# Performance work log

Hardware: AMD Instinct MI355X
Metric: run time of the kernel (lower is better)

## Reference

```python
import jax, jax.numpy as jnp
import numpy as np

N = 50000      # nodes
E = 800000     # edges (avg degree 16)
IN = 128       # in_channels
OUT = 128      # out_channels


def setup_inputs() -> dict:
    key = jax.random.key(0)
    k1, k2, k3 = jax.random.split(key, 3)
    x = jax.random.normal(k1, (N, IN), dtype=jnp.float32)
    edge_index = jax.random.randint(k2, (2, E), 0, N, dtype=jnp.int32)
    # GCNConv params: glorot-ish linear weight + zero bias
    W = jax.random.normal(k3, (IN, OUT), dtype=jnp.float32) / np.float32(np.sqrt(IN))
    b = jnp.zeros((OUT,), dtype=jnp.float32)
    return {"x": x, "W": W, "b": b, "edge_index": edge_index}


def reference(x, W, b, edge_index):
    n = x.shape[0]
    src, dst = edge_index[0], edge_index[1]
    # add self loops (GCNConv default add_self_loops=True)
    loop = jnp.arange(n, dtype=edge_index.dtype)
    src = jnp.concatenate([src, loop])
    dst = jnp.concatenate([dst, loop])
    # symmetric normalization: deg^{-1/2}[src] * deg^{-1/2}[dst], deg from dst (flow source_to_target)
    deg = jax.ops.segment_sum(jnp.ones_like(dst, dtype=x.dtype), dst, num_segments=n)
    dinv = jnp.where(deg > 0, jax.lax.rsqrt(jnp.maximum(deg, 1.0)), 0.0)
    norm = dinv[src] * dinv[dst]                     # [E+N]
    xw = x @ W                                       # [N, OUT] dense GEMM first (as GCNConv does)
    msg = xw[src] * norm[:, None]                    # [E+N, OUT] gather + scale
    out = jax.ops.segment_sum(msg, dst, num_segments=n)  # scatter-add aggregate
    return out + b
```

## Files before the change

kernel.cpp:

```cpp
#include <hip/hip_runtime.h>


constexpr int CH = 128;
constexpr int CHUNK = 4096;
constexpr int NCMAX = 256;

typedef __attribute__((ext_vector_type(8))) short short8;
typedef __attribute__((ext_vector_type(4))) float f32x4;

static __device__ __forceinline__ ushort f2bf(float f) {
    unsigned u = __float_as_uint(f);
    u += 0x7fff + ((u >> 16) & 1);
    return (ushort)(u >> 16);
}


__global__ __launch_bounds__(256) void hist_kernel(const int* __restrict__ dst,
                                                   int* __restrict__ h, int E, int nc) {
    __shared__ int hh[NCMAX];
    int t = threadIdx.x, b = blockIdx.x;
    for (int i = t; i < nc; i += 256) hh[i] = 0;
    __syncthreads();
    int s = b * CHUNK, e = min(E, s + CHUNK);
    for (int i = s + t; i < e; i += 256) atomicAdd(&hh[dst[i] >> 8], 1);
    __syncthreads();
    for (int i = t; i < nc; i += 256) h[b * nc + i] = hh[i];
}

__global__ __launch_bounds__(256) void colscan_cols(int* __restrict__ h,
        int* __restrict__ coltot, int nblk, int nc) {
    __shared__ int sm[256];
    int i = blockIdx.x;
    int t = threadIdx.x;
    int v = (t < nblk) ? h[t * nc + i] : 0;
    sm[t] = v;
    __syncthreads();
    #pragma unroll
    for (int d = 1; d < 256; d <<= 1) {
        int u = (t >= d) ? sm[t - d] : 0;
        __syncthreads();
        sm[t] += u;
        __syncthreads();
    }
    if (t < nblk) h[t * nc + i] = sm[t] - v;
    if (t == 255) coltot[i] = sm[255];
}

__global__ __launch_bounds__(256) void scan_bbase(const int* __restrict__ coltot,
        int* __restrict__ bbase, int nc) {
    __shared__ int sm[256];
    int t = threadIdx.x;
    int v = (t < nc) ? coltot[t] : 0;
    sm[t] = v;
    __syncthreads();
    #pragma unroll
    for (int d = 1; d < 256; d <<= 1) {
        int u = (t >= d) ? sm[t - d] : 0;
        __syncthreads();
        sm[t] += u;
        __syncthreads();
    }
    if (t < nc) bbase[t] = sm[t] - v;
    if (t == nc - 1) bbase[nc] = sm[t];
}

__global__ __launch_bounds__(256) void binscatter_kernel(const int* __restrict__ src,
        const int* __restrict__ dst, const int* __restrict__ h,
        const int* __restrict__ bbase, unsigned* __restrict__ ebuf, int E, int nc) {
    __shared__ int cur[NCMAX];
    int t = threadIdx.x, b = blockIdx.x;
    for (int i = t; i < nc; i += 256) cur[i] = h[b * nc + i] + bbase[i];
    __syncthreads();
    int s = b * CHUNK, e = min(E, s + CHUNK);
    for (int i = s + t; i < e; i += 256) {
        int d = dst[i];
        int pos = atomicAdd(&cur[d >> 8], 1);
        ebuf[pos] = (unsigned)src[i] | ((unsigned)(d & 255) << 16);
    }
}

__global__ __launch_bounds__(256) void bucket_csr_kernel(const unsigned* __restrict__ ebuf,
        const int* __restrict__ bbase, int* __restrict__ off, ushort* __restrict__ csr,
        float* __restrict__ dinv, int N) {
    __shared__ int hist[256], cur[256], sc[256];
    int t = threadIdx.x, k = blockIdx.x;
    int s = bbase[k], e = bbase[k + 1];
    hist[t] = 0;
    __syncthreads();
    for (int i = s + t; i < e; i += 256) atomicAdd(&hist[(ebuf[i] >> 16) & 255], 1);
    __syncthreads();
    int v = hist[t];
    sc[t] = v;
    __syncthreads();
    #pragma unroll
    for (int d = 1; d < 256; d <<= 1) {
        int u = (t >= d) ? sc[t - d] : 0;
        __syncthreads();
        sc[t] += u;
        __syncthreads();
    }
    int excl = sc[t] - v;
    int node = k * 256 + t;
    if (node <= N) off[node] = s + excl;
    if (node < N) dinv[node] = rsqrtf((float)(v + 1));
    cur[t] = s + excl;
    __syncthreads();
    for (int i = s + t; i < e; i += 256) {
        unsigned u = ebuf[i];
        int pos = atomicAdd(&cur[(u >> 16) & 255], 1);
        csr[pos] = (ushort)(u & 0xffffu);
    }
}


__global__ void pack_w(const float* __restrict__ W, ushort* __restrict__ Wp) {
    int tid = blockIdx.x * blockDim.x + threadIdx.x;
    if (tid >= 2048) return;
    int col = tid >> 4, chunk = tid & 15;
    ushort tmp[8];
    #pragma unroll
    for (int i = 0; i < 8; ++i)
        tmp[i] = f2bf(W[(size_t)(chunk * 8 + i) * CH + col]);
    int d = col * 16 + (chunk ^ (col & 7));
    *(uint4*)&Wp[(size_t)d * 8] = *(uint4*)tmp;
}


__global__ __launch_bounds__(256) void gemm_mfma(const float* __restrict__ x,
        const ushort* __restrict__ Wp, const float* __restrict__ dinv,
        ushort* __restrict__ xwd, int N) {
    __shared__ alignas(16) ushort Wlds[16384];
    int t = threadIdx.x;
    int wv = t >> 6, l = t & 63;
    int c15 = l & 15, kc = l >> 4;
    int row0 = blockIdx.x * 64 + wv * 16;
    int r = row0 + c15;
    bool valid = r < N;

    short8 af[4];
    #pragma unroll
    for (int ks = 0; ks < 4; ++ks) {
        float4 a0 = make_float4(0.f,0.f,0.f,0.f), a1 = a0;
        if (valid) {
            const float* p = x + (size_t)r * CH + ks * 32 + kc * 8;
            a0 = *(const float4*)p;
            a1 = *(const float4*)(p + 4);
        }
        short8 v;
        v[0]=f2bf(a0.x); v[1]=f2bf(a0.y); v[2]=f2bf(a0.z); v[3]=f2bf(a0.w);
        v[4]=f2bf(a1.x); v[5]=f2bf(a1.y); v[6]=f2bf(a1.z); v[7]=f2bf(a1.w);
        af[ks] = v;
    }

    #pragma unroll
    for (int i = 0; i < 8; ++i) {
        int idx = i * 256 + t;
        *(uint4*)&Wlds[idx * 8] = *(const uint4*)&Wp[idx * 8];
    }
    __syncthreads();

    f32x4 acc[8];
    #pragma unroll
    for (int ct = 0; ct < 8; ++ct) { f32x4 z = {0.f,0.f,0.f,0.f}; acc[ct] = z; }

    int swz = l & 7;
    #pragma unroll
    for (int ks = 0; ks < 4; ++ks) {
        #pragma unroll
        for (int ct = 0; ct < 8; ++ct) {
            int col = ct * 16 + c15;
            int idx16 = (col * 16 + ks * 4 + kc) ^ swz;
            short8 bfrag = *(const short8*)&Wlds[idx16 * 8];
            acc[ct] = __builtin_amdgcn_mfma_f32_16x16x32_bf16(af[ks], bfrag, acc[ct], 0, 0, 0);
        }
    }

    float dv[4];
    #pragma unroll
    for (int rr = 0; rr < 4; ++rr) {
        int row = row0 + kc * 4 + rr;
        dv[rr] = (row < N) ? dinv[row] : 0.f;
    }
    __syncthreads();

    ushort* bw = Wlds + wv * 2048;
    #pragma unroll
    for (int ct = 0; ct < 8; ++ct) {
        #pragma unroll
        for (int rr = 0; rr < 4; ++rr) {
            int row_local = kc * 4 + rr;
            bw[row_local * CH + ct * 16 + c15] = f2bf(acc[ct][rr] * dv[rr]);
        }
    }
    #pragma unroll
    for (int p = 0; p < 4; ++p) {
        int row_local = p * 4 + kc;
        int row = row0 + row_local;
        if (row < N) {
            uint4 vv = *(const uint4*)&bw[row_local * CH + c15 * 8];
            *(uint4*)&xwd[(size_t)row * CH + c15 * 8] = vv;
        }
    }
}


#define ACC8(v)                                    \
    acc[0] += __uint_as_float((v).x << 16);        \
    acc[1] += __uint_as_float((v).x & 0xffff0000u);\
    acc[2] += __uint_as_float((v).y << 16);        \
    acc[3] += __uint_as_float((v).y & 0xffff0000u);\
    acc[4] += __uint_as_float((v).z << 16);        \
    acc[5] += __uint_as_float((v).z & 0xffff0000u);\
    acc[6] += __uint_as_float((v).w << 16);        \
    acc[7] += __uint_as_float((v).w & 0xffff0000u);

__global__ __launch_bounds__(256) void agg_kernel(const ushort* __restrict__ xwd,
        const ushort* __restrict__ csr, const int* __restrict__ off,
        const float* __restrict__ dinv, const float* __restrict__ b,
        float* __restrict__ out, int N) {
    int t = threadIdx.x;
    int c15 = t & 15;
    int node = blockIdx.x * 16 + (t >> 4);
    if (node >= N) return;
    int s = off[node], e = off[node + 1];
    float acc[8] = {0.f,0.f,0.f,0.f,0.f,0.f,0.f,0.f};
    const ushort* base = xwd + c15 * 8;

    int j = s;
    for (; j + 4 <= e; j += 4) {
        int i0 = csr[j], i1 = csr[j + 1], i2 = csr[j + 2], i3 = csr[j + 3];
        uint4 v0 = *(const uint4*)(base + (size_t)i0 * CH);
        uint4 v1 = *(const uint4*)(base + (size_t)i1 * CH);
        uint4 v2 = *(const uint4*)(base + (size_t)i2 * CH);
        uint4 v3 = *(const uint4*)(base + (size_t)i3 * CH);
        ACC8(v0); ACC8(v1); ACC8(v2); ACC8(v3);
    }
    for (; j < e; ++j) {
        int i0 = csr[j];
        uint4 v = *(const uint4*)(base + (size_t)i0 * CH);
        ACC8(v);
    }
    {
        uint4 v = *(const uint4*)(base + (size_t)node * CH);
        ACC8(v);
    }
    float di = dinv[node];
    float4 b0 = *(const float4*)&b[c15 * 8];
    float4 b1 = *(const float4*)&b[c15 * 8 + 4];
    float4 o0, o1;
    o0.x = di * acc[0] + b0.x;  o0.y = di * acc[1] + b0.y;
    o0.z = di * acc[2] + b0.z;  o0.w = di * acc[3] + b0.w;
    o1.x = di * acc[4] + b1.x;  o1.y = di * acc[5] + b1.y;
    o1.z = di * acc[6] + b1.z;  o1.w = di * acc[7] + b1.w;
    float* op = out + (size_t)node * CH + c15 * 8;
    *(float4*)op = o0;
    *(float4*)(op + 4) = o1;
}


extern "C" void kernel_launch(void* const* d_in, const int* in_sizes, int n_in,
                              void* d_out, int out_size, void* d_ws, size_t ws_size,
                              hipStream_t stream) {
    const float* x  = (const float*)d_in[0];
    const float* Wm = (const float*)d_in[1];
    const float* b  = (const float*)d_in[2];
    const int*   ei = (const int*)d_in[3];
    int N = in_sizes[0] / CH;
    int E = in_sizes[3] / 2;
    const int* src = ei;
    const int* dst = ei + E;
    float* out = (float*)d_out;

    char* w = (char*)d_ws;
    auto alloc = [&](size_t bytes) {
        char* p = w;
        w += (bytes + 255) & ~(size_t)255;
        return p;
    };
    int nc = (N + 255) >> 8;
    int nblk = (E + CHUNK - 1) / CHUNK;

    ushort*   xwd  = (ushort*)alloc((size_t)N * CH * 2);
    unsigned* ebuf = (unsigned*)xwd;
    int*      off  = (int*)alloc((size_t)(N + 1) * 4);
    ushort*   csr  = (ushort*)alloc((size_t)E * 2);
    float*    dinv = (float*)alloc((size_t)N * 4);
    ushort*   Wp   = (ushort*)alloc((size_t)16384 * 2);
    int*      h    = (int*)alloc((size_t)nblk * nc * 4);
    int*      bbase= (int*)alloc((size_t)(nc + 1) * 4);
    int*      coltot=(int*)alloc((size_t)nc * 4);

    hist_kernel<<<nblk, 256, 0, stream>>>(dst, h, E, nc);
    colscan_cols<<<nc, 256, 0, stream>>>(h, coltot, nblk, nc);
    scan_bbase<<<1, 256, 0, stream>>>(coltot, bbase, nc);
    binscatter_kernel<<<nblk, 256, 0, stream>>>(src, dst, h, bbase, ebuf, E, nc);
    bucket_csr_kernel<<<nc, 256, 0, stream>>>(ebuf, bbase, off, csr, dinv, N);
    pack_w<<<8, 256, 0, stream>>>(Wm, Wp);
    gemm_mfma<<<(N + 63) / 64, 256, 0, stream>>>(x, Wp, dinv, xwd, N);
    agg_kernel<<<(N + 15) / 16, 256, 0, stream>>>(xwd, csr, off, dinv, b, out, N);
}
```

Measured before the change: 83.43 us.

## Fuse CSR build stages into one persistent kernel with grid barriers

```diff
diff --git a/kernel.cpp b/kernel.cpp
--- a/kernel.cpp
+++ b/kernel.cpp
@@ -2,8 +2,8 @@
 
 
 constexpr int CH = 128;
-constexpr int CHUNK = 4096;
 constexpr int NCMAX = 256;
+constexpr int GBLK = 256;
 
 typedef __attribute__((ext_vector_type(8))) short short8;
 typedef __attribute__((ext_vector_type(4))) float f32x4;
@@ -14,115 +14,119 @@
     return (ushort)(u >> 16);
 }
 
-
-__global__ __launch_bounds__(256) void hist_kernel(const int* __restrict__ dst,
-                                                   int* __restrict__ h, int E, int nc) {
-    __shared__ int hh[NCMAX];
+static __device__ __forceinline__ void grid_barrier(int* bar, int idx, int nblk) {
+    __syncthreads();
+    if (threadIdx.x == 0) {
+        __threadfence();
+        __hip_atomic_fetch_add(&bar[idx], 1, __ATOMIC_RELEASE, __HIP_MEMORY_SCOPE_AGENT);
+        while (__hip_atomic_load(&bar[idx], __ATOMIC_ACQUIRE, __HIP_MEMORY_SCOPE_AGENT) < nblk)
+            __builtin_amdgcn_s_sleep(2);
+    }
+    __syncthreads();
+}
+
+
+__global__ __launch_bounds__(256) void fused_csr(const int* __restrict__ src,
+        const int* __restrict__ dst, int* __restrict__ h, int* __restrict__ coltot,
+        int* __restrict__ bbase, unsigned* __restrict__ ebuf, int* __restrict__ off,
+        ushort* __restrict__ csr, float* __restrict__ dinv,
+        const float* __restrict__ Wm, ushort* __restrict__ Wp,
+        int* __restrict__ bar, int N, int E, int nc) {
+    __shared__ int sm[256];
+    __shared__ int cur[NCMAX];
+    __shared__ int hist2[256];
     int t = threadIdx.x, b = blockIdx.x;
-    for (int i = t; i < nc; i += 256) hh[i] = 0;
-    __syncthreads();
-    int s = b * CHUNK, e = min(E, s + CHUNK);
-    for (int i = s + t; i < e; i += 256) atomicAdd(&hh[dst[i] >> 8], 1);
-    __syncthreads();
-    for (int i = t; i < nc; i += 256) h[b * nc + i] = hh[i];
-}
-
-__global__ __launch_bounds__(256) void colscan_cols(int* __restrict__ h,
-        int* __restrict__ coltot, int nblk, int nc) {
-    __shared__ int sm[256];
-    int i = blockIdx.x;
-    int t = threadIdx.x;
-    int v = (t < nblk) ? h[t * nc + i] : 0;
-    sm[t] = v;
-    __syncthreads();
-    #pragma unroll
-    for (int d = 1; d < 256; d <<= 1) {
-        int u = (t >= d) ? sm[t - d] : 0;
-        __syncthreads();
-        sm[t] += u;
-        __syncthreads();
-    }
-    if (t < nblk) h[t * nc + i] = sm[t] - v;
-    if (t == 255) coltot[i] = sm[255];
-}
-
-__global__ __launch_bounds__(256) void scan_bbase(const int* __restrict__ coltot,
-        int* __restrict__ bbase, int nc) {
-    __shared__ int sm[256];
-    int t = threadIdx.x;
-    int v = (t < nc) ? coltot[t] : 0;
-    sm[t] = v;
-    __syncthreads();
-    #pragma unroll
-    for (int d = 1; d < 256; d <<= 1) {
-        int u = (t >= d) ? sm[t - d] : 0;
-        __syncthreads();
-        sm[t] += u;
-        __syncthreads();
-    }
-    if (t < nc) bbase[t] = sm[t] - v;
-    if (t == nc - 1) bbase[nc] = sm[t];
-}
-
-__global__ __launch_bounds__(256) void binscatter_kernel(const int* __restrict__ src,
-        const int* __restrict__ dst, const int* __restrict__ h,
-        const int* __restrict__ bbase, unsigned* __restrict__ ebuf, int E, int nc) {
-    __shared__ int cur[NCMAX];
-    int t = threadIdx.x, b = blockIdx.x;
-    for (int i = t; i < nc; i += 256) cur[i] = h[b * nc + i] + bbase[i];
-    __syncthreads();
-    int s = b * CHUNK, e = min(E, s + CHUNK);
-    for (int i = s + t; i < e; i += 256) {
+    int G = gridDim.x;
+    int chunk = (E + G - 1) / G;
+    int s0 = b * chunk, e0 = min(E, s0 + chunk);
+
+    for (int i = t; i < NCMAX; i += 256) cur[i] = 0;
+    __syncthreads();
+    for (int i = s0 + t; i < e0; i += 256) atomicAdd(&cur[dst[i] >> 8], 1);
+    __syncthreads();
+    for (int i = t; i < nc; i += 256) h[(size_t)i * G + b] = cur[i];
+    grid_barrier(bar, 0, G);
+
+    if (b < nc) {
+        int v = (t < G) ? h[(size_t)b * G + t] : 0;
+        sm[t] = v;
+        __syncthreads();
+        #pragma unroll
+        for (int d = 1; d < 256; d <<= 1) {
+            int u = (t >= d) ? sm[t - d] : 0;
+            __syncthreads();
+            sm[t] += u;
+            __syncthreads();
+        }
+        if (t < G) h[(size_t)b * G + t] = sm[t] - v;
+        if (t == 255) coltot[b] = sm[255];
+    }
+    grid_barrier(bar, 1, G);
+
+    if (b == 0) {
+        int v = (t < nc) ? coltot[t] : 0;
+        sm[t] = v;
+        __syncthreads();
+        #pragma unroll
+        for (int d = 1; d < 256; d <<= 1) {
+            int u = (t >= d) ? sm[t - d] : 0;
+            __syncthreads();
+            sm[t] += u;
+            __syncthreads();
+        }
+        if (t < nc) bbase[t] = sm[t] - v;
+        if (t == nc - 1) bbase[nc] = sm[t];
+    }
+    grid_barrier(bar, 2, G);
+
+    for (int i = t; i < nc; i += 256) cur[i] = h[(size_t)i * G + b] + bbase[i];
+    __syncthreads();
+    for (int i = s0 + t; i < e0; i += 256) {
         int d = dst[i];
         int pos = atomicAdd(&cur[d >> 8], 1);
         ebuf[pos] = (unsigned)src[i] | ((unsigned)(d & 255) << 16);
     }
-}
-
-__global__ __launch_bounds__(256) void bucket_csr_kernel(const unsigned* __restrict__ ebuf,
-        const int* __restrict__ bbase, int* __restrict__ off, ushort* __restrict__ csr,
-        float* __restrict__ dinv, int N) {
-    __shared__ int hist[256], cur[256], sc[256];
-    int t = threadIdx.x, k = blockIdx.x;
-    int s = bbase[k], e = bbase[k + 1];
-    hist[t] = 0;
-    __syncthreads();
-    for (int i = s + t; i < e; i += 256) atomicAdd(&hist[(ebuf[i] >> 16) & 255], 1);
-    __syncthreads();
-    int v = hist[t];
-    sc[t] = v;
-    __syncthreads();
-    #pragma unroll
-    for (int d = 1; d < 256; d <<= 1) {
-        int u = (t >= d) ? sc[t - d] : 0;
-        __syncthreads();
-        sc[t] += u;
-        __syncthreads();
-    }
-    int excl = sc[t] - v;
-    int node = k * 256 + t;
-    if (node <= N) off[node] = s + excl;
-    if (node < N) dinv[node] = rsqrtf((float)(v + 1));
-    cur[t] = s + excl;
-    __syncthreads();
-    for (int i = s + t; i < e; i += 256) {
-        unsigned u = ebuf[i];
-        int pos = atomicAdd(&cur[(u >> 16) & 255], 1);
-        csr[pos] = (ushort)(u & 0xffffu);
-    }
-}
-
-
-__global__ void pack_w(const float* __restrict__ W, ushort* __restrict__ Wp) {
-    int tid = blockIdx.x * blockDim.x + threadIdx.x;
-    if (tid >= 2048) return;
-    int col = tid >> 4, chunk = tid & 15;
-    ushort tmp[8];
-    #pragma unroll
-    for (int i = 0; i < 8; ++i)
-        tmp[i] = f2bf(W[(size_t)(chunk * 8 + i) * CH + col]);
-    int d = col * 16 + (chunk ^ (col & 7));
-    *(uint4*)&Wp[(size_t)d * 8] = *(uint4*)tmp;
+    grid_barrier(bar, 3, G);
+
+    if (b < nc) {
+        int s = bbase[b], e = bbase[b + 1];
+        hist2[t] = 0;
+        __syncthreads();
+        for (int i = s + t; i < e; i += 256) atomicAdd(&hist2[(ebuf[i] >> 16) & 255], 1);
+        __syncthreads();
+        int v = hist2[t];
+        sm[t] = v;
+        __syncthreads();
+        #pragma unroll
+        for (int d = 1; d < 256; d <<= 1) {
+            int u = (t >= d) ? sm[t - d] : 0;
+            __syncthreads();
+            sm[t] += u;
+            __syncthreads();
+        }
+        int excl = sm[t] - v;
+        int node = b * 256 + t;
+        if (node <= N) off[node] = s + excl;
+        if (node < N) dinv[node] = rsqrtf((float)(v + 1));
+        cur[t] = s + excl;
+        __syncthreads();
+        for (int i = s + t; i < e; i += 256) {
+            unsigned u = ebuf[i];
+            int pos = atomicAdd(&cur[(u >> 16) & 255], 1);
+            csr[pos] = (ushort)(u & 0xffffu);
+        }
+    } else if (b < nc + 8) {
+        int tid = (b - nc) * 256 + t;
+        if (tid < 2048) {
+            int col = tid >> 4, ch16 = tid & 15;
+            ushort tmp[8];
+            #pragma unroll
+            for (int i = 0; i < 8; ++i)
+                tmp[i] = f2bf(Wm[(size_t)(ch16 * 8 + i) * CH + col]);
+            int d = col * 16 + (ch16 ^ (col & 7));
+            *(uint4*)&Wp[(size_t)d * 8] = *(uint4*)tmp;
+        }
+    }
 }
 
 
@@ -203,16 +207,6 @@
     }
 }
 
-
-#define ACC8(v)                                    \
-    acc[0] += __uint_as_float((v).x << 16);        \
-    acc[1] += __uint_as_float((v).x & 0xffff0000u);\
-    acc[2] += __uint_as_float((v).y << 16);        \
-    acc[3] += __uint_as_float((v).y & 0xffff0000u);\
-    acc[4] += __uint_as_float((v).z << 16);        \
-    acc[5] += __uint_as_float((v).z & 0xffff0000u);\
-    acc[6] += __uint_as_float((v).w << 16);        \
-    acc[7] += __uint_as_float((v).w & 0xffff0000u);
 
 __global__ __launch_bounds__(256) void agg_kernel(const ushort* __restrict__ xwd,
         const ushort* __restrict__ csr, const int* __restrict__ off,
@@ -226,23 +220,41 @@
     float acc[8] = {0.f,0.f,0.f,0.f,0.f,0.f,0.f,0.f};
     const ushort* base = xwd + c15 * 8;
 
-    int j = s;
-    for (; j + 4 <= e; j += 4) {
-        int i0 = csr[j], i1 = csr[j + 1], i2 = csr[j + 2], i3 = csr[j + 3];
-        uint4 v0 = *(const uint4*)(base + (size_t)i0 * CH);
-        uint4 v1 = *(const uint4*)(base + (size_t)i1 * CH);
-        uint4 v2 = *(const uint4*)(base + (size_t)i2 * CH);
-        uint4 v3 = *(const uint4*)(base + (size_t)i3 * CH);
-        ACC8(v0); ACC8(v1); ACC8(v2); ACC8(v3);
-    }
-    for (; j < e; ++j) {
-        int i0 = csr[j];
-        uint4 v = *(const uint4*)(base + (size_t)i0 * CH);
-        ACC8(v);
+    int last = e - 1;
+    for (int j = s; j < e; j += 8) {
+        int idx[8]; float m[8];
+        #pragma unroll
+        for (int k = 0; k < 8; ++k) {
+            int jj = j + k;
+            idx[k] = csr[min(jj, last)];
+            m[k] = (jj <= last) ? 1.0f : 0.0f;
+        }
+        uint4 v[8];
+        #pragma unroll
+        for (int k = 0; k < 8; ++k)
+            v[k] = *(const uint4*)(base + (size_t)idx[k] * CH);
+        #pragma unroll
+        for (int k = 0; k < 8; ++k) {
+            acc[0] += m[k] * __uint_as_float(v[k].x << 16);
+            acc[1] += m[k] * __uint_as_float(v[k].x & 0xffff0000u);
+            acc[2] += m[k] * __uint_as_float(v[k].y << 16);
+            acc[3] += m[k] * __uint_as_float(v[k].y & 0xffff0000u);
+            acc[4] += m[k] * __uint_as_float(v[k].z << 16);
+            acc[5] += m[k] * __uint_as_float(v[k].z & 0xffff0000u);
+            acc[6] += m[k] * __uint_as_float(v[k].w << 16);
+            acc[7] += m[k] * __uint_as_float(v[k].w & 0xffff0000u);
+        }
     }
     {
         uint4 v = *(const uint4*)(base + (size_t)node * CH);
-        ACC8(v);
+        acc[0] += __uint_as_float(v.x << 16);
+        acc[1] += __uint_as_float(v.x & 0xffff0000u);
+        acc[2] += __uint_as_float(v.y << 16);
+        acc[3] += __uint_as_float(v.y & 0xffff0000u);
+        acc[4] += __uint_as_float(v.z << 16);
+        acc[5] += __uint_as_float(v.z & 0xffff0000u);
+        acc[6] += __uint_as_float(v.w << 16);
+        acc[7] += __uint_as_float(v.w & 0xffff0000u);
     }
     float di = dinv[node];
     float4 b0 = *(const float4*)&b[c15 * 8];
@@ -278,7 +290,6 @@
         return p;
     };
     int nc = (N + 255) >> 8;
-    int nblk = (E + CHUNK - 1) / CHUNK;
 
     ushort*   xwd  = (ushort*)alloc((size_t)N * CH * 2);
     unsigned* ebuf = (unsigned*)xwd;
@@ -286,16 +297,14 @@
     ushort*   csr  = (ushort*)alloc((size_t)E * 2);
     float*    dinv = (float*)alloc((size_t)N * 4);
     ushort*   Wp   = (ushort*)alloc((size_t)16384 * 2);
-    int*      h    = (int*)alloc((size_t)nblk * nc * 4);
+    int*      h    = (int*)alloc((size_t)nc * GBLK * 4);
     int*      bbase= (int*)alloc((size_t)(nc + 1) * 4);
     int*      coltot=(int*)alloc((size_t)nc * 4);
-
-    hist_kernel<<<nblk, 256, 0, stream>>>(dst, h, E, nc);
-    colscan_cols<<<nc, 256, 0, stream>>>(h, coltot, nblk, nc);
-    scan_bbase<<<1, 256, 0, stream>>>(coltot, bbase, nc);
-    binscatter_kernel<<<nblk, 256, 0, stream>>>(src, dst, h, bbase, ebuf, E, nc);
-    bucket_csr_kernel<<<nc, 256, 0, stream>>>(ebuf, bbase, off, csr, dinv, N);
-    pack_w<<<8, 256, 0, stream>>>(Wm, Wp);
+    int*      bar  = (int*)alloc(4 * sizeof(int));
+
+    hipMemsetAsync(bar, 0, 4 * sizeof(int), stream);
+    fused_csr<<<GBLK, 256, 0, stream>>>(src, dst, h, coltot, bbase, ebuf, off, csr,
+                                        dinv, Wm, Wp, bar, N, E, nc);
     gemm_mfma<<<(N + 63) / 64, 256, 0, stream>>>(x, Wp, dinv, xwd, N);
     agg_kernel<<<(N + 15) / 16, 256, 0, stream>>>(xwd, csr, off, dinv, b, out, N);
 }
```

New measurement: 171.2 us. 2.05x slower.
